# Kernel optimization log

Hardware: AMD Instinct MI355X
Metric: run time of the kernel (lower is better)

## Reference

```python
import jax, jax.numpy as jnp
import numpy as np

ALPHA = 0.1
BETA = float(np.log(1.0 / 4.0 + 1.0))  # lambda_=1, layer=4

N_NODES = 50000
N_EDGES = 600000
D = 128


def setup_inputs() -> dict:
    key = jax.random.key(0)
    k1, k2, k3, k4, k5 = jax.random.split(key, 5)
    feat = jax.random.normal(k1, (N_NODES, D), dtype=jnp.float32)
    feat_0 = jax.random.normal(k2, (N_NODES, D), dtype=jnp.float32)
    weight1 = jax.random.normal(k3, (D, D), dtype=jnp.float32)  # nn.init.normal_
    bias = jnp.zeros((D,), dtype=jnp.float32)
    src = jax.random.randint(k4, (N_EDGES,), 0, N_NODES, dtype=jnp.int32)
    dst = jax.random.randint(k5, (N_EDGES,), 0, N_NODES, dtype=jnp.int32)
    return {"feat": feat, "feat_0": feat_0, "weight1": weight1, "bias": bias,
            "src": src, "dst": dst}


def reference(feat, feat_0, weight1, bias, src, dst):
    n = feat.shape[0]
    # symmetric normalization: D^{-1/2} A_hat D^{-1/2} using in-degrees, clamped at 1
    deg = jax.ops.segment_sum(jnp.ones(dst.shape[0], dtype=feat.dtype), dst,
                              num_segments=n)
    norm = jnp.clip(deg, 1.0)[:, None] ** -0.5  # [N, 1]
    h = feat * norm
    agg = jax.ops.segment_sum(h[src], dst, num_segments=n)  # copy_u + sum
    agg = agg * norm
    # initial residual blend (torch does feat.add_(feat_0) in-place -> blended h
    # feeds both terms of the addmm)
    h = agg * (1.0 - ALPHA) + feat_0 * ALPHA
    # identity mapping: (1-beta)*h + beta*(h @ W1), plus bias
    rst = (1.0 - BETA) * h + BETA * (h @ weight1) + bias
    return rst
```

## Files before the change

### kernel.cpp

```cpp
#include <hip/hip_runtime.h>

static constexpr int   N_NODES = 50000;
static constexpr int   N_EDGES = 600000;
static constexpr int   D       = 128;
static constexpr int   CAP     = 64;
static constexpr float ALPHA   = 0.1f;
static constexpr float BETA    = 0.22314355131420976f;
static constexpr float OMB     = 1.0f - BETA;

static constexpr int TM = 32;
static constexpr int NT = (N_NODES + TM - 1) / TM;

__device__ __forceinline__ unsigned int f2bf(float f) {
    unsigned int u = __float_as_uint(f);
    return (u + 0x7FFFu + ((u >> 16) & 1u)) >> 16;
}
__device__ __forceinline__ float bf2f(unsigned int b) {
    return __uint_as_float(b << 16);
}
__device__ __forceinline__ float deg2norm(int d) {
    return rsqrtf(fmaxf((float)d, 1.0f));
}

__global__ void conv_kernel(const float* __restrict__ feat,
                            unsigned short* __restrict__ featb,
                            int* __restrict__ cnt) {
    const int tid = blockIdx.x * blockDim.x + threadIdx.x;
    if (tid * 4 < N_NODES)
        *reinterpret_cast<int4*>(cnt + tid * 4) = make_int4(0, 0, 0, 0);
    const size_t e0 = (size_t)tid * 16;
    if (e0 < (size_t)N_NODES * D) {
        const float* p = feat + e0;
        #pragma unroll
        for (int q = 0; q < 2; ++q) {
            float4 a = *reinterpret_cast<const float4*>(p + q * 8);
            float4 b = *reinterpret_cast<const float4*>(p + q * 8 + 4);
            uint4 o;
            o.x = f2bf(a.x) | (f2bf(a.y) << 16);
            o.y = f2bf(a.z) | (f2bf(a.w) << 16);
            o.z = f2bf(b.x) | (f2bf(b.y) << 16);
            o.w = f2bf(b.z) | (f2bf(b.w) << 16);
            *reinterpret_cast<uint4*>(featb + e0 + q * 8) = o;
        }
    }
}

__global__ void fill_kernel(const int* __restrict__ src, const int* __restrict__ dst,
                            int* __restrict__ cnt, int* __restrict__ slots) {
    const int tid = blockIdx.x * blockDim.x + threadIdx.x;
    if (tid < N_EDGES) {
        int s = src[tid];
        int d = dst[tid];
        int p = atomicAdd(&cnt[d], 1);
        if (p < CAP) slots[d * CAP + p] = s;
    }
}

__global__ __launch_bounds__(256) void gather_kernel(
    const unsigned short* __restrict__ featb, const int* __restrict__ slots,
    const int* __restrict__ cnt_arr, float* __restrict__ agg) {
    const int node = blockIdx.x * 4 + (threadIdx.x >> 6);
    const int lane = threadIdx.x & 63;
    const int half = lane >> 5;
    const int l32  = lane & 31;
    if (node >= N_NODES) return;
    const int base = node * CAP;
    const int cnt  = min(cnt_arr[node], CAP);
    const unsigned short* __restrict__ fcol = featb + (size_t)l32 * 4;

    int   s_l = 0;
    float n_l = 0.0f;
    if (lane < cnt) {
        s_l = slots[base + lane];
        n_l = deg2norm(cnt_arr[s_l]);
    }

    float4 acc = make_float4(0.f, 0.f, 0.f, 0.f);
    const int nb = (cnt + 7) >> 3;
    for (int b = 0; b < nb; ++b) {
        const int j = b * 8 + half;
        int   s0 = __shfl(s_l, j);      float n0 = __shfl(n_l, j);
        int   s1 = __shfl(s_l, j + 2);  float n1 = __shfl(n_l, j + 2);
        int   s2 = __shfl(s_l, j + 4);  float n2 = __shfl(n_l, j + 4);
        int   s3 = __shfl(s_l, j + 6);  float n3 = __shfl(n_l, j + 6);
        ushort4 u0 = *reinterpret_cast<const ushort4*>(fcol + (size_t)s0 * D);
        ushort4 u1 = *reinterpret_cast<const ushort4*>(fcol + (size_t)s1 * D);
        ushort4 u2 = *reinterpret_cast<const ushort4*>(fcol + (size_t)s2 * D);
        ushort4 u3 = *reinterpret_cast<const ushort4*>(fcol + (size_t)s3 * D);
        acc.x += bf2f(u0.x)*n0 + bf2f(u1.x)*n1 + bf2f(u2.x)*n2 + bf2f(u3.x)*n3;
        acc.y += bf2f(u0.y)*n0 + bf2f(u1.y)*n1 + bf2f(u2.y)*n2 + bf2f(u3.y)*n3;
        acc.z += bf2f(u0.z)*n0 + bf2f(u1.z)*n1 + bf2f(u2.z)*n2 + bf2f(u3.z)*n3;
        acc.w += bf2f(u0.w)*n0 + bf2f(u1.w)*n1 + bf2f(u2.w)*n2 + bf2f(u3.w)*n3;
    }
    acc.x += __shfl_xor(acc.x, 32);
    acc.y += __shfl_xor(acc.y, 32);
    acc.z += __shfl_xor(acc.z, 32);
    acc.w += __shfl_xor(acc.w, 32);
    if (half == 0)
        *reinterpret_cast<float4*>(agg + (size_t)node * D + l32 * 4) = acc;
}

__global__ __launch_bounds__(256, 4) void final_kernel(
    const float* __restrict__ feat_0,
    const float* __restrict__ W,
    const float* __restrict__ bias,
    const int* __restrict__ cnt_arr,
    float* __restrict__ out)
{
    __shared__ float h_sh[TM * D];

    const int t    = threadIdx.x;
    const int row0 = blockIdx.x * TM;

    #pragma unroll
    for (int i = 0; i < 4; ++i) {
        int idx  = (i * 256 + t) * 4;
        int r    = idx >> 7;
        int c    = idx & 127;
        int node = row0 + r;
        float4 h = make_float4(0.f, 0.f, 0.f, 0.f);
        if (node < N_NODES) {
            float nm = deg2norm(cnt_arr[node]) * (1.0f - ALPHA);
            float4 a  = *reinterpret_cast<const float4*>(out    + (size_t)node * D + c);
            float4 f0 = *reinterpret_cast<const float4*>(feat_0 + (size_t)node * D + c);
            h.x = a.x * nm + f0.x * ALPHA;
            h.y = a.y * nm + f0.y * ALPHA;
            h.z = a.z * nm + f0.z * ALPHA;
            h.w = a.w * nm + f0.w * ALPHA;
        }
        *reinterpret_cast<float4*>(&h_sh[idx]) = h;
    }
    __syncthreads();

    const int c0 = (t & 31) * 4;
    const int r0 = (t >> 5) * 4;
    const float* __restrict__ Wc = W + c0;

    float4 acc[4];
    #pragma unroll
    for (int j = 0; j < 4; ++j) acc[j] = make_float4(0.f, 0.f, 0.f, 0.f);

    #pragma unroll 1
    for (int kk = 0; kk < 128; kk += 4) {
        float4 wv[4];
        #pragma unroll
        for (int ki = 0; ki < 4; ++ki)
            wv[ki] = *reinterpret_cast<const float4*>(Wc + (size_t)(kk + ki) * D);
        float4 hv[4];
        #pragma unroll
        for (int j = 0; j < 4; ++j)
            hv[j] = *reinterpret_cast<const float4*>(&h_sh[(r0 + j) * D + kk]);
        #pragma unroll
        for (int ki = 0; ki < 4; ++ki) {
            #pragma unroll
            for (int j = 0; j < 4; ++j) {
                float hj = (ki == 0) ? hv[j].x : (ki == 1) ? hv[j].y
                         : (ki == 2) ? hv[j].z : hv[j].w;
                acc[j].x += hj * wv[ki].x;
                acc[j].y += hj * wv[ki].y;
                acc[j].z += hj * wv[ki].z;
                acc[j].w += hj * wv[ki].w;
            }
        }
    }

    const float4 b4 = *reinterpret_cast<const float4*>(bias + c0);
    #pragma unroll
    for (int j = 0; j < 4; ++j) {
        int node = row0 + r0 + j;
        if (node < N_NODES) {
            float4 h = *reinterpret_cast<const float4*>(&h_sh[(r0 + j) * D + c0]);
            float4 o;
            o.x = OMB * h.x + BETA * acc[j].x + b4.x;
            o.y = OMB * h.y + BETA * acc[j].y + b4.y;
            o.z = OMB * h.z + BETA * acc[j].z + b4.z;
            o.w = OMB * h.w + BETA * acc[j].w + b4.w;
            *reinterpret_cast<float4*>(out + (size_t)node * D + c0) = o;
        }
    }
}

extern "C" void kernel_launch(void* const* d_in, const int* in_sizes, int n_in,
                              void* d_out, int out_size, void* d_ws, size_t ws_size,
                              hipStream_t stream) {
    const float* feat   = (const float*)d_in[0];
    const float* feat_0 = (const float*)d_in[1];
    const float* W      = (const float*)d_in[2];
    const float* bias   = (const float*)d_in[3];
    const int*   src    = (const int*)d_in[4];
    const int*   dst    = (const int*)d_in[5];
    float*       out    = (float*)d_out;

    char* ws = (char*)d_ws;
    int*   cnt   = (int*)ws;            ws += (size_t)N_NODES * 4;
    int*   slots = (int*)ws;            ws += (size_t)N_NODES * CAP * 4;
    unsigned short* featb = (unsigned short*)ws;

    conv_kernel<<<(N_NODES * (D / 16) + 255) / 256, 256, 0, stream>>>(feat, featb, cnt);

    fill_kernel<<<(N_EDGES + 255) / 256, 256, 0, stream>>>(src, dst, cnt, slots);

    gather_kernel<<<(N_NODES + 3) / 4, 256, 0, stream>>>(featb, slots, cnt, out);

    final_kernel<<<NT, 256, 0, stream>>>(feat_0, W, bias, cnt, out);
}
```

Measured before the change: 200.4 us.

## Use bf16 MFMA for the dense W1 matmul with pre-transposed bf16 weights

Converts W1 to a transposed bf16 copy inside the conversion kernel and replaces the scalar FP32 FMA GEMM in final_kernel with MFMA 16x16x32 bf16 instructions. The row tile grows to 64 nodes and the shared tile is padded to avoid bank conflicts. The h operand is rounded to bf16 before the matmul, which lowers precision. The output stores become scalar per column rather than float4, which may be less coalesced.

```diff
diff --git a/kernel.cpp b/kernel.cpp
--- a/kernel.cpp
+++ b/kernel.cpp
@@ -8,8 +8,12 @@
 static constexpr float BETA    = 0.22314355131420976f;
 static constexpr float OMB     = 1.0f - BETA;
 
-static constexpr int TM = 32;
-static constexpr int NT = (N_NODES + TM - 1) / TM;
+static constexpr int TMF = 64;
+static constexpr int NTF = (N_NODES + TMF - 1) / TMF;
+static constexpr int HP  = 132;
+
+typedef __attribute__((ext_vector_type(8))) short short8;
+typedef __attribute__((ext_vector_type(4))) float f32x4;
 
 __device__ __forceinline__ unsigned int f2bf(float f) {
     unsigned int u = __float_as_uint(f);
@@ -24,10 +28,23 @@
 
 __global__ void conv_kernel(const float* __restrict__ feat,
                             unsigned short* __restrict__ featb,
+                            const float* __restrict__ W,
+                            unsigned short* __restrict__ wbt,
                             int* __restrict__ cnt) {
     const int tid = blockIdx.x * blockDim.x + threadIdx.x;
     if (tid * 4 < N_NODES)
         *reinterpret_cast<int4*>(cnt + tid * 4) = make_int4(0, 0, 0, 0);
+    if (tid * 8 < D * D) {
+        const int c  = (tid * 8) >> 7;
+        const int k0 = (tid * 8) & 127;
+        unsigned short w8[8];
+        #pragma unroll
+        for (int j = 0; j < 8; ++j)
+            w8[j] = (unsigned short)f2bf(W[(size_t)(k0 + j) * D + c]);
+        #pragma unroll
+        for (int j = 0; j < 8; ++j)
+            wbt[(size_t)c * D + k0 + j] = w8[j];
+    }
     const size_t e0 = (size_t)tid * 16;
     if (e0 < (size_t)N_NODES * D) {
         const float* p = feat + e0;
@@ -100,20 +117,20 @@
         *reinterpret_cast<float4*>(agg + (size_t)node * D + l32 * 4) = acc;
 }
 
-__global__ __launch_bounds__(256, 4) void final_kernel(
+__global__ __launch_bounds__(256, 2) void final_kernel(
     const float* __restrict__ feat_0,
-    const float* __restrict__ W,
+    const unsigned short* __restrict__ wbt,
     const float* __restrict__ bias,
     const int* __restrict__ cnt_arr,
     float* __restrict__ out)
 {
-    __shared__ float h_sh[TM * D];
+    __shared__ float h_sh[TMF * HP];
 
     const int t    = threadIdx.x;
-    const int row0 = blockIdx.x * TM;
-
-    #pragma unroll
-    for (int i = 0; i < 4; ++i) {
+    const int row0 = blockIdx.x * TMF;
+
+    #pragma unroll
+    for (int i = 0; i < 8; ++i) {
         int idx  = (i * 256 + t) * 4;
         int r    = idx >> 7;
         int c    = idx & 127;
@@ -128,54 +145,72 @@
             h.z = a.z * nm + f0.z * ALPHA;
             h.w = a.w * nm + f0.w * ALPHA;
         }
-        *reinterpret_cast<float4*>(&h_sh[idx]) = h;
+        *reinterpret_cast<float4*>(&h_sh[r * HP + c]) = h;
     }
     __syncthreads();
 
-    const int c0 = (t & 31) * 4;
-    const int r0 = (t >> 5) * 4;
-    const float* __restrict__ Wc = W + c0;
-
-    float4 acc[4];
-    #pragma unroll
-    for (int j = 0; j < 4; ++j) acc[j] = make_float4(0.f, 0.f, 0.f, 0.f);
-
-    #pragma unroll 1
-    for (int kk = 0; kk < 128; kk += 4) {
-        float4 wv[4];
-        #pragma unroll
-        for (int ki = 0; ki < 4; ++ki)
-            wv[ki] = *reinterpret_cast<const float4*>(Wc + (size_t)(kk + ki) * D);
-        float4 hv[4];
-        #pragma unroll
-        for (int j = 0; j < 4; ++j)
-            hv[j] = *reinterpret_cast<const float4*>(&h_sh[(r0 + j) * D + kk]);
-        #pragma unroll
-        for (int ki = 0; ki < 4; ++ki) {
+    const int wave = t >> 6;
+    const int lane = t & 63;
+    const int lrow = lane & 15;
+    const int lgrp = lane >> 4;
+    const int cb   = wave * 32;
+
+    short8 bfrag[2][4];
+    #pragma unroll
+    for (int ct = 0; ct < 2; ++ct) {
+        const int col = cb + ct * 16 + lrow;
+        #pragma unroll
+        for (int kb = 0; kb < 4; ++kb)
+            bfrag[ct][kb] = *reinterpret_cast<const short8*>(
+                wbt + (size_t)col * D + kb * 32 + lgrp * 8);
+    }
+
+    f32x4 acc[4][2];
+    #pragma unroll
+    for (int rt = 0; rt < 4; ++rt)
+        #pragma unroll
+        for (int ct = 0; ct < 2; ++ct)
+            acc[rt][ct] = (f32x4){0.f, 0.f, 0.f, 0.f};
+
+    #pragma unroll
+    for (int rt = 0; rt < 4; ++rt) {
+        const float* hp = &h_sh[(rt * 16 + lrow) * HP];
+        short8 afrag[4];
+        #pragma unroll
+        for (int kb = 0; kb < 4; ++kb) {
+            float4 x = *reinterpret_cast<const float4*>(hp + kb * 32 + lgrp * 8);
+            float4 y = *reinterpret_cast<const float4*>(hp + kb * 32 + lgrp * 8 + 4);
+            short8 a;
+            a[0] = (short)f2bf(x.x); a[1] = (short)f2bf(x.y);
+            a[2] = (short)f2bf(x.z); a[3] = (short)f2bf(x.w);
+            a[4] = (short)f2bf(y.x); a[5] = (short)f2bf(y.y);
+            a[6] = (short)f2bf(y.z); a[7] = (short)f2bf(y.w);
+            afrag[kb] = a;
+        }
+        #pragma unroll
+        for (int ct = 0; ct < 2; ++ct)
             #pragma unroll
-            for (int j = 0; j < 4; ++j) {
-                float hj = (ki == 0) ? hv[j].x : (ki == 1) ? hv[j].y
-                         : (ki == 2) ? hv[j].z : hv[j].w;
-                acc[j].x += hj * wv[ki].x;
-                acc[j].y += hj * wv[ki].y;
-                acc[j].z += hj * wv[ki].z;
-                acc[j].w += hj * wv[ki].w;
+            for (int kb = 0; kb < 4; ++kb)
+                acc[rt][ct] = __builtin_amdgcn_mfma_f32_16x16x32_bf16(
+                    afrag[kb], bfrag[ct][kb], acc[rt][ct], 0, 0, 0);
+    }
+
+    #pragma unroll
+    for (int ct = 0; ct < 2; ++ct) {
+        const int col = cb + ct * 16 + lrow;
+        const float bv = bias[col];
+        #pragma unroll
+        for (int rt = 0; rt < 4; ++rt) {
+            #pragma unroll
+            for (int reg = 0; reg < 4; ++reg) {
+                const int lr   = rt * 16 + lgrp * 4 + reg;
+                const int node = row0 + lr;
+                if (node < N_NODES) {
+                    float h = h_sh[lr * HP + col];
+                    out[(size_t)node * D + col] =
+                        OMB * h + BETA * acc[rt][ct][reg] + bv;
+                }
             }
-        }
-    }
-
-    const float4 b4 = *reinterpret_cast<const float4*>(bias + c0);
-    #pragma unroll
-    for (int j = 0; j < 4; ++j) {
-        int node = row0 + r0 + j;
-        if (node < N_NODES) {
-            float4 h = *reinterpret_cast<const float4*>(&h_sh[(r0 + j) * D + c0]);
-            float4 o;
-            o.x = OMB * h.x + BETA * acc[j].x + b4.x;
-            o.y = OMB * h.y + BETA * acc[j].y + b4.y;
-            o.z = OMB * h.z + BETA * acc[j].z + b4.z;
-            o.w = OMB * h.w + BETA * acc[j].w + b4.w;
-            *reinterpret_cast<float4*>(out + (size_t)node * D + c0) = o;
         }
     }
 }
@@ -194,13 +229,15 @@
     char* ws = (char*)d_ws;
     int*   cnt   = (int*)ws;            ws += (size_t)N_NODES * 4;
     int*   slots = (int*)ws;            ws += (size_t)N_NODES * CAP * 4;
-    unsigned short* featb = (unsigned short*)ws;
-
-    conv_kernel<<<(N_NODES * (D / 16) + 255) / 256, 256, 0, stream>>>(feat, featb, cnt);
+    unsigned short* featb = (unsigned short*)ws;  ws += (size_t)N_NODES * D * 2;
+    unsigned short* wbt   = (unsigned short*)ws;
+
+    conv_kernel<<<(N_NODES * (D / 16) + 255) / 256, 256, 0, stream>>>(
+        feat, featb, W, wbt, cnt);
 
     fill_kernel<<<(N_EDGES + 255) / 256, 256, 0, stream>>>(src, dst, cnt, slots);
 
     gather_kernel<<<(N_NODES + 3) / 4, 256, 0, stream>>>(featb, slots, cnt, out);
 
-    final_kernel<<<NT, 256, 0, stream>>>(feat_0, W, bias, cnt, out);
-}
+    final_kernel<<<NTF, 256, 0, stream>>>(feat_0, wbt, bias, cnt, out);
+}
```

Measured after the change: 181.0 us. 1.11x faster.
